# Performance work log

Hardware: AMD Instinct MI355X
Metric: run time of the kernel (lower is better)

The kernel has to match this reference:

```python
import jax, jax.numpy as jnp
import numpy as np

VOCAB = 50257

def setup_inputs() -> dict:
    key = jax.random.key(0)
    k1, k2, k3, k4 = jax.random.split(key, 4)
    B, T, S = 4, 4096, 8192  # batch, target_len, seq_len
    tokens = jax.random.randint(k1, (B, T), 0, VOCAB, dtype=jnp.int64)
    batch_input_ids = jax.random.randint(k2, (2, B, S), 0, VOCAB, dtype=jnp.int64)
    candidate_tokens = jax.random.randint(k3, (B, T), 0, VOCAB, dtype=jnp.int64)
    candidate_scores = jax.random.normal(k4, (B, T), dtype=jnp.float32)
    unmask_count = 4096
    return {"tokens": tokens, "batch_input_ids": batch_input_ids,
            "candidate_tokens": candidate_tokens, "candidate_scores": candidate_scores,
            "unmask_count": unmask_count}

def reference(tokens, batch_input_ids, candidate_tokens, candidate_scores, unmask_count):
    flat_scores = candidate_scores.reshape(-1)            # [N]
    flat_cand = candidate_tokens.reshape(-1)              # [N]
    flat_tok = tokens.reshape(-1)                         # [N]
    N = flat_scores.shape[0]
    idx = jnp.arange(N)
    # Stable 'better-than' matrix: strictly higher score, or equal score with lower index.
    better = (flat_scores[None, :] > flat_scores[:, None]) | (
        (flat_scores[None, :] == flat_scores[:, None]) & (idx[None, :] < idx[:, None]))
    rank = jnp.sum(better, axis=1)                        # [N] int
    selected = rank < jnp.asarray(unmask_count, dtype=rank.dtype)
    updated_flat = jnp.where(selected, flat_cand, flat_tok)
    updated_tokens = updated_flat.reshape(tokens.shape).astype(jnp.int64)
    S = batch_input_ids.shape[-1]
    T = tokens.shape[-1]
    upd = batch_input_ids
    upd = upd.at[0:1, :, S - T:S].set(updated_tokens[None])
    upd = upd.at[1:2, :, 0:T].set(updated_tokens[None])
    return updated_tokens, upd.astype(jnp.int64)
```

## Files before the change

### kernel.cpp

```cpp
#include <hip/hip_runtime.h>

#define NTOK 16384
#define BQ 4
#define TQ 4096
#define SQ 8192
#define BLK 1024
#define PER_T 16
#define NSLOT 32
#define HPAD 33

__device__ __forceinline__ unsigned score_key(float s) {
    unsigned u = __float_as_uint(s);
    if ((u << 1) == 0u) u = 0u;
    return (u & 0x80000000u) ? ~u : (u | 0x80000000u);
}

__global__ __launch_bounds__(BLK) void token_update_kernel(
    const float* __restrict__ scores,
    const int* __restrict__ cand,
    const int* __restrict__ tok,
    const int* __restrict__ bids,
    const int* __restrict__ kptr,
    int* __restrict__ out0,
    int* __restrict__ out1)
{
    const int tid = threadIdx.x;

    if (blockIdx.x > 0) {
        int g  = (blockIdx.x - 1) * BLK + tid;
        int o4 = g << 2;
        int c  = o4 >> 12;
        int b  = c & 3, plane = c >> 2;
        int off = o4 & 4095;
        int addr = (plane == 0) ? (b * SQ + off)
                                : (BQ * SQ + b * SQ + TQ + off);
        *(int4*)(out1 + addr) = *(const int4*)(bids + addr);
        return;
    }

    __shared__ int hist[256][HPAD];
    __shared__ int cnt[256];
    __shared__ int scanbuf[BLK];
    __shared__ unsigned s_prefix;
    __shared__ int s_krem, s_E;

    const int K = kptr[0];
    const bool none = (K <= 0);
    const bool all  = (K >= NTOK);
    const bool run  = !none && !all;
    const int slot = tid & (NSLOT - 1);

    for (int t = tid; t < 256 * HPAD; t += BLK) ((int*)hist)[t] = 0;
    if (tid == 0) { s_prefix = 0u; s_krem = K; s_E = K; }
    __syncthreads();

    float sv[PER_T];
    #pragma unroll
    for (int t = 0; t < PER_T; ++t) sv[t] = scores[t * BLK + tid];
    unsigned key[PER_T];
    #pragma unroll
    for (int t = 0; t < PER_T; ++t) {
        unsigned k = score_key(sv[t]);
        key[t] = k;
        atomicAdd(&hist[k >> 24][slot], 1);
    }
    __syncthreads();

    for (int level = 0; level < 4; ++level) {
        if (tid < 256) {
            int s = 0;
            #pragma unroll
            for (int j = 0; j < NSLOT; ++j) s += hist[tid][j];
            cnt[tid] = s;
        }
        __syncthreads();

        if (run && tid < 64) {
            int c0 = cnt[4 * tid], c1 = cnt[4 * tid + 1];
            int c2 = cnt[4 * tid + 2], c3 = cnt[4 * tid + 3];
            int T = c0 + c1 + c2 + c3;
            int incl = T;
            #pragma unroll
            for (int off = 1; off < 64; off <<= 1) {
                int o = __shfl_down(incl, off, 64);
                if (tid + off < 64) incl += o;
            }
            int suf4 = incl - T;
            int suf3 = suf4 + c3;
            int suf2 = suf3 + c2;
            int suf1 = suf2 + c1;
            int suf0 = suf1 + c0;
            int krem = s_krem;
            int shift = 24 - 8 * level;
            int sufs[5] = {suf0, suf1, suf2, suf3, suf4};
            int cs[4] = {c0, c1, c2, c3};
            #pragma unroll
            for (int j = 0; j < 4; ++j) {
                if (sufs[j] >= krem && sufs[j + 1] < krem) {
                    s_prefix = s_prefix | ((unsigned)(4 * tid + j) << shift);
                    s_krem = krem - sufs[j + 1];
                    s_E = cs[j];
                }
            }
        }
        __syncthreads();

        if (level < 3) {
            for (int t = tid; t < 256 * HPAD; t += BLK) ((int*)hist)[t] = 0;
            __syncthreads();
            if (run) {
                unsigned pref = s_prefix;
                int msh = 24 - 8 * level;
                int shift = msh - 8;
                #pragma unroll
                for (int t = 0; t < PER_T; ++t) {
                    unsigned k = key[t];
                    if ((k >> msh) == (pref >> msh))
                        atomicAdd(&hist[(k >> shift) & 255][slot], 1);
                }
            }
            __syncthreads();
        }
    }

    const unsigned Tstar = s_prefix;
    const int R = s_krem, E = s_E;

    if (!run || R == E) {
        #pragma unroll
        for (int t = 0; t < PER_T; ++t) {
            int i = t * BLK + tid;
            bool sel = none ? false : (all ? true : (key[t] >= Tstar));
            int v = sel ? cand[i] : tok[i];
            int b = i >> 12, tt = i & 4095;
            out0[i] = v;
            out1[b * SQ + (SQ - TQ) + tt] = v;
            out1[BQ * SQ + b * SQ + tt] = v;
        }
    } else {
        unsigned ck[PER_T];
        int cntEq = 0;
        #pragma unroll
        for (int j = 0; j < PER_T; ++j) {
            unsigned k = score_key(scores[tid * PER_T + j]);
            ck[j] = k;
            cntEq += (k == Tstar) ? 1 : 0;
        }
        scanbuf[tid] = cntEq;
        __syncthreads();
        for (int off = 1; off < BLK; off <<= 1) {
            int v = scanbuf[tid];
            int add = (tid >= off) ? scanbuf[tid - off] : 0;
            __syncthreads();
            scanbuf[tid] = v + add;
            __syncthreads();
        }
        int running = scanbuf[tid] - cntEq;
        for (int j = 0; j < PER_T; ++j) {
            int i = tid * PER_T + j;
            unsigned k = ck[j];
            bool sel;
            if (k > Tstar) sel = true;
            else if (k == Tstar) { sel = (running < R); ++running; }
            else sel = false;
            int v = sel ? cand[i] : tok[i];
            int b = i >> 12, tt = i & 4095;
            out0[i] = v;
            out1[b * SQ + (SQ - TQ) + tt] = v;
            out1[BQ * SQ + b * SQ + tt] = v;
        }
    }
}

extern "C" void kernel_launch(void* const* d_in, const int* in_sizes, int n_in,
                              void* d_out, int out_size, void* d_ws, size_t ws_size,
                              hipStream_t stream) {
    const int*   tok    = (const int*)d_in[0];
    const int*   bids   = (const int*)d_in[1];
    const int*   cand   = (const int*)d_in[2];
    const float* scores = (const float*)d_in[3];
    const int*   kptr   = (const int*)d_in[4];

    int* out0 = (int*)d_out;
    int* out1 = out0 + NTOK;

    token_update_kernel<<<9, BLK, 0, stream>>>(scores, cand, tok, bids, kptr, out0, out1);
}
```

Baseline: 70.50 us.

## Split selection into bitmask kernel and parallel vectorized gather/scatter epilogue

The single-block selection kernel now only computes a selection bitmask (via wavefront ballots or packed per-thread masks) into workspace. A second kernel then spreads the candidate/token merge and the three output writes across many blocks with int4 vector loads and stores. This moves the memory-bound tail off the single serial block, at the cost of an extra launch and a workspace round trip. It also skips the histogram atomics when no radix search is needed.

Result: slower. 73.93 us (+4.9%).

```diff
diff --git a/kernel.cpp b/kernel.cpp
--- a/kernel.cpp
+++ b/kernel.cpp
@@ -15,13 +15,11 @@
     return (u & 0x80000000u) ? ~u : (u | 0x80000000u);
 }
 
-__global__ __launch_bounds__(BLK) void token_update_kernel(
+__global__ __launch_bounds__(BLK) void select_kernel(
     const float* __restrict__ scores,
-    const int* __restrict__ cand,
-    const int* __restrict__ tok,
     const int* __restrict__ bids,
     const int* __restrict__ kptr,
-    int* __restrict__ out0,
+    unsigned long long* __restrict__ bm,
     int* __restrict__ out1)
 {
     const int tid = threadIdx.x;
@@ -54,15 +52,12 @@
     if (tid == 0) { s_prefix = 0u; s_krem = K; s_E = K; }
     __syncthreads();
 
-    float sv[PER_T];
-    #pragma unroll
-    for (int t = 0; t < PER_T; ++t) sv[t] = scores[t * BLK + tid];
     unsigned key[PER_T];
     #pragma unroll
     for (int t = 0; t < PER_T; ++t) {
-        unsigned k = score_key(sv[t]);
+        unsigned k = score_key(scores[t * BLK + tid]);
         key[t] = k;
-        atomicAdd(&hist[k >> 24][slot], 1);
+        if (run) atomicAdd(&hist[k >> 24][slot], 1);
     }
     __syncthreads();
 
@@ -129,13 +124,9 @@
     if (!run || R == E) {
         #pragma unroll
         for (int t = 0; t < PER_T; ++t) {
-            int i = t * BLK + tid;
             bool sel = none ? false : (all ? true : (key[t] >= Tstar));
-            int v = sel ? cand[i] : tok[i];
-            int b = i >> 12, tt = i & 4095;
-            out0[i] = v;
-            out1[b * SQ + (SQ - TQ) + tt] = v;
-            out1[BQ * SQ + b * SQ + tt] = v;
+            unsigned long long m = __ballot(sel);
+            if ((tid & 63) == 0) bm[t * 16 + (tid >> 6)] = m;
         }
     } else {
         unsigned ck[PER_T];
@@ -156,20 +147,49 @@
             __syncthreads();
         }
         int running = scanbuf[tid] - cntEq;
+        unsigned mask16 = 0;
         for (int j = 0; j < PER_T; ++j) {
-            int i = tid * PER_T + j;
             unsigned k = ck[j];
             bool sel;
             if (k > Tstar) sel = true;
             else if (k == Tstar) { sel = (running < R); ++running; }
             else sel = false;
-            int v = sel ? cand[i] : tok[i];
-            int b = i >> 12, tt = i & 4095;
-            out0[i] = v;
-            out1[b * SQ + (SQ - TQ) + tt] = v;
-            out1[BQ * SQ + b * SQ + tt] = v;
-        }
-    }
+            if (sel) mask16 |= (1u << j);
+        }
+        __syncthreads();
+        scanbuf[tid] = (int)mask16;
+        __syncthreads();
+        if (tid < 256) {
+            unsigned long long W = 0;
+            #pragma unroll
+            for (int j = 0; j < 4; ++j)
+                W |= ((unsigned long long)((unsigned)scanbuf[4 * tid + j] & 0xFFFFu)) << (16 * j);
+            bm[tid] = W;
+        }
+    }
+}
+
+__global__ __launch_bounds__(256) void epilogue_kernel(
+    const int* __restrict__ cand,
+    const int* __restrict__ tok,
+    const unsigned long long* __restrict__ bm,
+    int* __restrict__ out0,
+    int* __restrict__ out1)
+{
+    int q = blockIdx.x * 256 + threadIdx.x;
+    int i = q << 2;
+    unsigned bits = (unsigned)(bm[i >> 6] >> (i & 60)) & 0xFu;
+    int4 c = ((const int4*)cand)[q];
+    int4 t = ((const int4*)tok)[q];
+    int4 v;
+    v.x = (bits & 1u) ? c.x : t.x;
+    v.y = (bits & 2u) ? c.y : t.y;
+    v.z = (bits & 4u) ? c.z : t.z;
+    v.w = (bits & 8u) ? c.w : t.w;
+    ((int4*)out0)[q] = v;
+    int b = i >> 12, tt = i & 4095;
+    *(int4*)(out1 + b * SQ + (SQ - TQ) + tt) = v;
+    *(int4*)(out1 + BQ * SQ + b * SQ + tt) = v;
 }
 
 extern "C" void kernel_launch(void* const* d_in, const int* in_sizes, int n_in,
@@ -183,6 +203,8 @@
 
     int* out0 = (int*)d_out;
     int* out1 = out0 + NTOK;
-
-    token_update_kernel<<<9, BLK, 0, stream>>>(scores, cand, tok, bids, kptr, out0, out1);
-}
+    unsigned long long* bm = (unsigned long long*)d_ws;
+
+    select_kernel<<<9, BLK, 0, stream>>>(scores, bids, kptr, bm, out1);
+    epilogue_kernel<<<NTOK / 4 / 256, 256, 0, stream>>>(cand, tok, bm, out0, out1);
+}
```
